# Kernel optimization log

Measured on AMD Instinct MI355X. Metric: run time of the kernel, lower is better.

## Reference

```python
import jax, jax.numpy as jnp
import numpy as np

DELTA_PULL = 0.5
DELTA_PUSH = 1.5
ALPHA, BETA, GAMMA = 1.0, 1.0, 0.001
M, E = 2_000_000, 32
NUM_IDS = 65  # labels 0..64; 0 = background


def setup_inputs() -> dict:
    key = jax.random.key(0)
    k1, k2 = jax.random.split(key)
    embeddings = jax.random.normal(k1, (M, E), dtype=jnp.float32)
    instance_labels = jax.random.randint(k2, (M,), 0, NUM_IDS, dtype=jnp.int64)
    return {"embeddings": embeddings, "instance_labels": instance_labels}


def reference(embeddings, instance_labels):
    # Foreground mask; background (label 0) points are excluded from every term.
    fg = instance_labels > 0
    labels = jnp.where(fg, instance_labels, 0).astype(jnp.int32)
    w = fg.astype(embeddings.dtype)  # [M]

    # Per-instance means via one fused segment-sum (replaces Python loop over ids).
    sums = jax.ops.segment_sum(embeddings * w[:, None], labels, num_segments=NUM_IDS)  # [C+1,E]
    counts = jax.ops.segment_sum(w, labels, num_segments=NUM_IDS)                       # [C+1]
    present = (counts > 0).at[0].set(False)  # slot 0 is background
    safe_counts = jnp.maximum(counts, 1.0)
    means = sums / safe_counts[:, None]  # [C+1,E]
    C = jnp.sum(present)
    Cf = jnp.maximum(C, 1).astype(embeddings.dtype)

    # Pull loss: per-point distance to own instance mean, hinged, per-instance mean, then mean over instances.
    diff_pt = embeddings - means[labels]
    d2_pt = jnp.sum(diff_pt * diff_pt, axis=1)
    dist_pt = jnp.sqrt(jnp.where(d2_pt > 0, d2_pt, 1.0))
    dist_pt = jnp.where(d2_pt > 0, dist_pt, 0.0)
    pull_pt = jnp.maximum(dist_pt - DELTA_PULL, 0.0) ** 2 * w
    pull_per_inst = jax.ops.segment_sum(pull_pt, labels, num_segments=NUM_IDS) / safe_counts
    pull_loss = jnp.sum(jnp.where(present, pull_per_inst, 0.0)) / Cf

    # Push loss: vectorized O(C^2) pairwise mean distances with upper-triangular mask.
    dm = means[:, None, :] - means[None, :, :]           # [C+1,C+1,E]
    d2 = jnp.sum(dm * dm, axis=-1)                        # [C+1,C+1]
    iu = jnp.triu(jnp.ones((NUM_IDS, NUM_IDS), bool), k=1)
    pairmask = iu & present[:, None] & present[None, :]
    pd = jnp.sqrt(jnp.where(pairmask, d2, 1.0))
    push = jnp.where(pairmask, jnp.maximum(2.0 * DELTA_PUSH - pd, 0.0) ** 2, 0.0)
    n_pairs = jnp.sum(pairmask)
    push_loss = jnp.where(
        n_pairs > 0,
        jnp.sum(push) / jnp.maximum(n_pairs, 1).astype(embeddings.dtype),
        0.0,
    )

    # Regularizer: mean norm of present instance means.
    mn2 = jnp.sum(means * means, axis=-1)
    mnorm = jnp.sqrt(jnp.where(present, mn2, 1.0))
    reg_loss = jnp.sum(jnp.where(present, mnorm, 0.0)) / Cf

    total = ALPHA * pull_loss + BETA * push_loss + GAMMA * reg_loss
    # If there are no foreground points, loss is 0 (matches torch early-return).
    total = jnp.where(C > 0, total, 0.0)
    return total
```

## Files before the change

### kernel.cpp

```cpp
#include <hip/hip_runtime.h>

#define NUM_IDS 65
#define EDIM 32
#define NSUM (NUM_IDS * EDIM)
#define NTOT (NSUM + NUM_IDS)
#define LPAD 33
#define R36 36
#define CP (NUM_IDS * R36)

#define WS_SUMS    0
#define WS_PULLACC 2148
#define WS_PART    2176

#define DPPI(x, ctrl) __builtin_amdgcn_update_dpp(0, (x), (ctrl), 0xF, 0xF, true)

__device__ __forceinline__ void gload4(const float4* p, float4& d) {
    asm volatile("global_load_dwordx4 %0, %1, off" : "=v"(d) : "v"(p));
}
__device__ __forceinline__ void gload1(const int* p, int& d) {
    asm volatile("global_load_dword %0, %1, off" : "=v"(d) : "v"(p));
}
__device__ __forceinline__ void waitN() {
    asm volatile("s_waitcnt vmcnt(4)" ::: "memory");
    __builtin_amdgcn_sched_barrier(0);
}
__device__ __forceinline__ void wait0() {
    asm volatile("s_waitcnt vmcnt(0)" ::: "memory");
    __builtin_amdgcn_sched_barrier(0);
}

__global__ void k0_zero(float* __restrict__ ws) {
    int i = blockIdx.x * 256 + threadIdx.x;
    if (i < NTOT) ws[WS_SUMS + i] = 0.f;
    if (i == 0) ws[WS_PULLACC] = 0.f;
}

__global__ __launch_bounds__(256) void k1_reduce(const float4* __restrict__ emb4,
                                                 const int* __restrict__ lab,
                                                 float* __restrict__ ws,
                                                 int M, int nb1, int nit, int atomic_mode) {
    __shared__ float ls[4 * CP];
    const int t = threadIdx.x;
    const int wave = t >> 6, lane = t & 63;
    const int s = lane & 7;
    const int c = lane >> 3;
    float* my = ls + wave * CP;
    for (int j = t; j < 4 * CP; j += 256) ls[j] = 0.f;
    __syncthreads();

    const long Mm1 = (long)M - 1;
    const long STR = (long)nb1 * 32;
    const long p0 = (long)blockIdx.x * 32 + wave * 8 + s;
    const int lp1 = lane + 1;
    int cntreg = 0;
    const int negkey = -64 - s;
    const int e1 = (s ^ 1) < s, e2 = (s ^ 2) < s, e3 = (s ^ 3) < s,
              e4 = (s ^ 4) < s, e5 = (s ^ 5) < s, e6 = (s ^ 6) < s, e7 = (s ^ 7) < s;

    auto ISSUE = [&](int j, int& L, float4& v) {
        long p = p0 + (long)j * STR;
        long pc = p < Mm1 ? p : Mm1;
        gload1(lab + pc, L);
        gload4(emb4 + pc * 8 + c, v);
    };
    auto PROC = [&](int j, int L, float4 v) {
        const bool inb = (p0 + (long)j * STR) < (long)M;
        const bool act = inb && (L > 0);
        int x0 = act ? L : negkey;
        int x1 = DPPI(x0, 0xB1);
        int x2 = DPPI(x0, 0x4E);
        int x3 = DPPI(x1, 0x4E);
        int x4 = DPPI(x0, 0x124);
        int x5 = DPPI(x1, 0x124);
        int x6 = DPPI(x2, 0x124);
        int x7 = DPPI(x3, 0x124);
        cntreg += (x0 == lp1) + (x1 == lp1) + (x2 == lp1) + (x3 == lp1)
                + (x4 == lp1) + (x5 == lp1) + (x6 == lp1) + (x7 == lp1);
        int ne = (e1 & (x1 == x0)) + (e2 & (x2 == x0)) + (e3 & (x3 == x0))
               + (e4 & (x4 == x0)) + (e5 & (x5 == x0)) + (e6 & (x6 == x0))
               + (e7 & (x7 == x0));
        const int off = (act ? L : 0) * R36 + c * 4;
        if (act && ne == 0) {
            float4 o = *(float4*)(my + off);
            o.x += v.x; o.y += v.y; o.z += v.z; o.w += v.w;
            *(float4*)(my + off) = o;
        }
        if (__ballot(act && ne > 0)) {
            #pragma unroll 1
            for (int r = 1; r < 8; ++r) {
                if (!__ballot(act && ne == r)) break;
                if (act && ne == r) {
                    float4 o = *(float4*)(my + off);
                    o.x += v.x; o.y += v.y; o.z += v.z; o.w += v.w;
                    *(float4*)(my + off) = o;
                }
            }
        }
    };

    int LA, LB, LC; float4 VA, VB, VC;
    ISSUE(0, LA, VA); ISSUE(1, LB, VB);
    for (int i = 0; i < nit; i += 3) {
        ISSUE(i + 2, LC, VC); waitN(); PROC(i, LA, VA);
        ISSUE(i + 3, LA, VA); waitN(); PROC(i + 1, LB, VB);
        ISSUE(i + 4, LB, VB); waitN(); PROC(i + 2, LC, VC);
    }
    wait0();

    my[lp1 * R36 + 32] += (float)cntreg;
    __syncthreads();

    for (int j = t; j < NTOT; j += 256) {
        int off = (j < NSUM) ? ((j >> 5) * R36 + (j & 31))
                             : ((j - NSUM) * R36 + 32);
        float v = ls[off] + ls[CP + off] + ls[2 * CP + off] + ls[3 * CP + off];
        if (atomic_mode) {
            if (v != 0.f) atomicAdd(&ws[WS_SUMS + j], v);
        } else {
            ws[WS_PART + (size_t)blockIdx.x * NTOT + j] = v;
        }
    }
}

__global__ __launch_bounds__(256) void k2_reduce_partials(float* __restrict__ ws, int nb1) {
    const int t = threadIdx.x;
    const int jl = t & 31, bl = t >> 5;
    const int j = blockIdx.x * 32 + jl;
    const float* part = ws + WS_PART;
    float acc = 0.f;
    if (j < NTOT) {
        int b = bl;
        for (; b + 56 < nb1; b += 64) {
            float v0 = part[(size_t)(b +  0) * NTOT + j];
            float v1 = part[(size_t)(b +  8) * NTOT + j];
            float v2 = part[(size_t)(b + 16) * NTOT + j];
            float v3 = part[(size_t)(b + 24) * NTOT + j];
            float v4 = part[(size_t)(b + 32) * NTOT + j];
            float v5 = part[(size_t)(b + 40) * NTOT + j];
            float v6 = part[(size_t)(b + 48) * NTOT + j];
            float v7 = part[(size_t)(b + 56) * NTOT + j];
            acc += ((v0 + v1) + (v2 + v3)) + ((v4 + v5) + (v6 + v7));
        }
        for (; b < nb1; b += 8) acc += part[(size_t)b * NTOT + j];
    }
    __shared__ float red[256];
    red[t] = acc;
    __syncthreads();
    for (int sd = 128; sd >= 32; sd >>= 1) {
        if (t < sd) red[t] += red[t + sd];
        __syncthreads();
    }
    if (t < 32) {
        int jj = blockIdx.x * 32 + t;
        if (jj < NTOT) ws[WS_SUMS + jj] = red[t];
    }
    if (blockIdx.x == 0 && t == 0) ws[WS_PULLACC] = 0.f;
}

__global__ __launch_bounds__(256) void k4_pull(const float4* __restrict__ emb4,
                                               const int* __restrict__ lab,
                                               float* __restrict__ ws,
                                               int M, int nb4) {
    __shared__ float lmean[NUM_IDS * LPAD];
    __shared__ float lcoef[NUM_IDS];
    __shared__ float lpull[NUM_IDS];
    __shared__ float red[NUM_IDS];
    const int t = threadIdx.x;
    for (int j = t; j < NSUM; j += 256) {
        int cc = j >> 5;
        lmean[cc * LPAD + (j & 31)] = ws[WS_SUMS + j] / fmaxf(ws[WS_SUMS + NSUM + cc], 1.f);
    }
    if (t < NUM_IDS) {
        float cv = ws[WS_SUMS + NSUM + t];
        lcoef[t] = (t > 0 && cv > 0.f) ? (1.f / fmaxf(cv, 1.f)) : 0.f;
        lpull[t] = 0.f;
    }
    __syncthreads();

    const int c = t & 7;
    const long stride = (long)nb4 * 32;
    const long start = (long)blockIdx.x * 32 + (t >> 3);

    auto LD = [&](long p, int& L, float4& v) {
        if (p < M) { L = lab[p]; v = emb4[p * 8 + c]; }
        else       { L = 0; v = make_float4(0.f, 0.f, 0.f, 0.f); }
    };
    auto PR = [&](int L, float4 v) {
        float d2 = 0.f;
        if (L > 0) {
            int bse = L * LPAD + c * 4;
            float dx = v.x - lmean[bse + 0];
            float dy = v.y - lmean[bse + 1];
            float dz = v.z - lmean[bse + 2];
            float dw = v.w - lmean[bse + 3];
            d2 = dx * dx + dy * dy + dz * dz + dw * dw;
        }
        d2 += __shfl_xor(d2, 1);
        d2 += __shfl_xor(d2, 2);
        d2 += __shfl_xor(d2, 4);
        if (c == 0 && L > 0 && d2 > 0.f) {
            float dist = sqrtf(d2);
            float h = fmaxf(dist - 0.5f, 0.f);
            atomicAdd(&lpull[L], h * h);
        }
    };

    int L0, L1;
    float4 v0, v1;
    long pA = start;
    LD(pA, L0, v0);
    while (pA < M) {
        const long pB = pA + stride;
        LD(pB, L1, v1);
        PR(L0, v0);
        const long pA2 = pB + stride;
        LD(pA2, L0, v0);
        PR(L1, v1);
        pA = pA2;
    }
    __syncthreads();
    if (t < NUM_IDS) red[t] = lpull[t] * lcoef[t];
    __syncthreads();
    if (t == 0) {
        float sacc = 0.f;
        for (int cc = 1; cc < NUM_IDS; ++cc) sacc += red[cc];
        atomicAdd(&ws[WS_PULLACC], sacc);
    }
}

__global__ __launch_bounds__(256) void k5_final(float* __restrict__ ws,
                                                float* __restrict__ out) {
    __shared__ float lmean[NUM_IDS * LPAD];
    __shared__ int   lpres[NUM_IDS];
    __shared__ float red[256];
    __shared__ float red2[256];
    const int t = threadIdx.x;

    if (t < NUM_IDS) {
        float cv = ws[WS_SUMS + NSUM + t];
        lpres[t] = (t > 0 && cv > 0.f) ? 1 : 0;
    }
    for (int j = t; j < NSUM; j += 256) {
        int cc = j >> 5;
        lmean[cc * LPAD + (j & 31)] = ws[WS_SUMS + j] / fmaxf(ws[WS_SUMS + NSUM + cc], 1.f);
    }
    __syncthreads();

    float psum = 0.f;
    for (int pi = t; pi < 2080; pi += 256) {
        int i = 0, rem = pi;
        while (rem >= NUM_IDS - 1 - i) { rem -= NUM_IDS - 1 - i; ++i; }
        int jj = i + 1 + rem;
        if (lpres[i] && lpres[jj]) {
            float d2 = 0.f;
            #pragma unroll
            for (int e = 0; e < EDIM; ++e) {
                float d = lmean[i * LPAD + e] - lmean[jj * LPAD + e];
                d2 += d * d;
            }
            float pd = sqrtf(d2);
            float h = fmaxf(3.0f - pd, 0.f);
            psum += h * h;
        }
    }
    float rsum = 0.f;
    if (t < NUM_IDS && lpres[t]) {
        float m2 = 0.f;
        #pragma unroll
        for (int e = 0; e < EDIM; ++e) { float m = lmean[t * LPAD + e]; m2 += m * m; }
        rsum = sqrtf(m2);
    }
    red[t] = psum; red2[t] = rsum;
    __syncthreads();
    for (int sd = 128; sd > 0; sd >>= 1) {
        if (t < sd) { red[t] += red[t + sd]; red2[t] += red2[t + sd]; }
        __syncthreads();
    }
    if (t == 0) {
        int C = 0;
        for (int cc = 1; cc < NUM_IDS; ++cc) C += lpres[cc];
        float Cf = fmaxf((float)C, 1.f);
        long np = (long)C * (C - 1) / 2;
        float push = (np > 0) ? red[0] / (float)np : 0.f;
        float reg  = red2[0] / Cf;
        float total = 0.f;
        if (C > 0) total = ws[WS_PULLACC] / Cf + push + 0.001f * reg;
        out[0] = total;
    }
}

extern "C" void kernel_launch(void* const* d_in, const int* in_sizes, int n_in,
                              void* d_out, int out_size, void* d_ws, size_t ws_size,
                              hipStream_t stream) {
    const float4* emb4 = (const float4*)d_in[0];
    const int* lab = (const int*)d_in[1];
    float* ws = (float*)d_ws;
    float* out = (float*)d_out;
    const int M = in_sizes[1];

    long ws_floats = (long)(ws_size / 4);
    long avail = ws_floats - WS_PART - 64;
    int nb1 = (int)(avail / NTOT);
    if (nb1 > 1024) nb1 = 1024;
    int atomic_mode = (nb1 < 8) ? 1 : 0;
    if (atomic_mode) {
        nb1 = 1024;
        k0_zero<<<dim3(9), dim3(256), 0, stream>>>(ws);
    }
    long str1 = (long)nb1 * 32;
    int nit1 = (int)((M + str1 - 1) / str1);
    nit1 = ((nit1 + 2) / 3) * 3;

    k1_reduce<<<dim3(nb1), dim3(256), 0, stream>>>(emb4, lab, ws, M, nb1, nit1, atomic_mode);
    if (!atomic_mode)
        k2_reduce_partials<<<dim3((NTOT + 31) / 32), dim3(256), 0, stream>>>(ws, nb1);
    const int nb4 = 2048;
    k4_pull<<<dim3(nb4), dim3(256), 0, stream>>>(emb4, lab, ws, M, nb4);
    k5_final<<<dim3(1), dim3(256), 0, stream>>>(ws, out);
}
```

Before: 135.3 us.

## Software-pipeline pull kernel with asm loads, DPP reduction and nontemporal hints

Rewrites the pull kernel's main loop as a three-deep software pipeline. Loads are issued with inline asm and explicit vmcnt waits, which replaces the compiler-scheduled two-stage loop with bounds branches. The 8-lane distance reduction moves from shfl_xor to DPP, and means are stored with stride 36 so each lane reads a float4 from LDS. Embedding loads in both streaming kernels gain the nt hint to reduce cache pollution. The trade-off is more register pressure, and nt may stop the second pass over the embeddings from reusing data left in cache by the first.

```diff
diff --git a/kernel.cpp b/kernel.cpp
--- a/kernel.cpp
+++ b/kernel.cpp
@@ -4,7 +4,6 @@
 #define EDIM 32
 #define NSUM (NUM_IDS * EDIM)
 #define NTOT (NSUM + NUM_IDS)
-#define LPAD 33
 #define R36 36
 #define CP (NUM_IDS * R36)
 
@@ -14,8 +13,8 @@
 
 #define DPPI(x, ctrl) __builtin_amdgcn_update_dpp(0, (x), (ctrl), 0xF, 0xF, true)
 
-__device__ __forceinline__ void gload4(const float4* p, float4& d) {
-    asm volatile("global_load_dwordx4 %0, %1, off" : "=v"(d) : "v"(p));
+__device__ __forceinline__ void gload4nt(const float4* p, float4& d) {
+    asm volatile("global_load_dwordx4 %0, %1, off nt" : "=v"(d) : "v"(p));
 }
 __device__ __forceinline__ void gload1(const int* p, int& d) {
     asm volatile("global_load_dword %0, %1, off" : "=v"(d) : "v"(p));
@@ -61,7 +60,7 @@
         long p = p0 + (long)j * STR;
         long pc = p < Mm1 ? p : Mm1;
         gload1(lab + pc, L);
-        gload4(emb4 + pc * 8 + c, v);
+        gload4nt(emb4 + pc * 8 + c, v);
     };
     auto PROC = [&](int j, int L, float4 v) {
         const bool inb = (p0 + (long)j * STR) < (long)M;
@@ -160,15 +159,17 @@
 __global__ __launch_bounds__(256) void k4_pull(const float4* __restrict__ emb4,
                                                const int* __restrict__ lab,
                                                float* __restrict__ ws,
-                                               int M, int nb4) {
-    __shared__ float lmean[NUM_IDS * LPAD];
+                                               int M, int nb4, int nit) {
+    __shared__ float lmean[NUM_IDS * R36];
     __shared__ float lcoef[NUM_IDS];
     __shared__ float lpull[NUM_IDS];
     __shared__ float red[NUM_IDS];
     const int t = threadIdx.x;
+    const int lane = t & 63;
+    const int s = lane >> 3, c = lane & 7;
     for (int j = t; j < NSUM; j += 256) {
         int cc = j >> 5;
-        lmean[cc * LPAD + (j & 31)] = ws[WS_SUMS + j] / fmaxf(ws[WS_SUMS + NSUM + cc], 1.f);
+        lmean[cc * R36 + (j & 31)] = ws[WS_SUMS + j] / fmaxf(ws[WS_SUMS + NSUM + cc], 1.f);
     }
     if (t < NUM_IDS) {
         float cv = ws[WS_SUMS + NSUM + t];
@@ -177,47 +178,42 @@
     }
     __syncthreads();
 
-    const int c = t & 7;
-    const long stride = (long)nb4 * 32;
-    const long start = (long)blockIdx.x * 32 + (t >> 3);
-
-    auto LD = [&](long p, int& L, float4& v) {
-        if (p < M) { L = lab[p]; v = emb4[p * 8 + c]; }
-        else       { L = 0; v = make_float4(0.f, 0.f, 0.f, 0.f); }
+    const long Mm1 = (long)M - 1;
+    const long STR = (long)nb4 * 32;
+    const long p0 = (long)blockIdx.x * 32 + (t >> 6) * 8 + s;
+
+    auto ISSUE = [&](int j, int& L, float4& v) {
+        long p = p0 + (long)j * STR;
+        long pc = p < Mm1 ? p : Mm1;
+        gload1(lab + pc, L);
+        gload4nt(emb4 + pc * 8 + c, v);
     };
-    auto PR = [&](int L, float4 v) {
-        float d2 = 0.f;
-        if (L > 0) {
-            int bse = L * LPAD + c * 4;
-            float dx = v.x - lmean[bse + 0];
-            float dy = v.y - lmean[bse + 1];
-            float dz = v.z - lmean[bse + 2];
-            float dw = v.w - lmean[bse + 3];
-            d2 = dx * dx + dy * dy + dz * dz + dw * dw;
-        }
-        d2 += __shfl_xor(d2, 1);
-        d2 += __shfl_xor(d2, 2);
-        d2 += __shfl_xor(d2, 4);
-        if (c == 0 && L > 0 && d2 > 0.f) {
+    auto PROC = [&](int j, int L, float4 v) {
+        const bool inb = (p0 + (long)j * STR) < (long)M;
+        const bool act = inb && (L > 0);
+        const float4 mu = *(const float4*)(lmean + L * R36 + c * 4);
+        float dx = v.x - mu.x, dy = v.y - mu.y, dz = v.z - mu.z, dw = v.w - mu.w;
+        float d2 = act ? (dx * dx + dy * dy + dz * dz + dw * dw) : 0.f;
+        int bb;
+        bb = DPPI(__float_as_int(d2), 0xB1); d2 += __int_as_float(bb);
+        bb = DPPI(__float_as_int(d2), 0x4E); d2 += __int_as_float(bb);
+        bb = DPPI(DPPI(__float_as_int(d2), 0x141), 0x1B);
+        d2 += __int_as_float(bb);
+        if (c == 0 && act && d2 > 0.f) {
             float dist = sqrtf(d2);
             float h = fmaxf(dist - 0.5f, 0.f);
             atomicAdd(&lpull[L], h * h);
         }
     };
 
-    int L0, L1;
-    float4 v0, v1;
-    long pA = start;
-    LD(pA, L0, v0);
-    while (pA < M) {
-        const long pB = pA + stride;
-        LD(pB, L1, v1);
-        PR(L0, v0);
-        const long pA2 = pB + stride;
-        LD(pA2, L0, v0);
-        PR(L1, v1);
-        pA = pA2;
-    }
+    int LA, LB, LC; float4 VA, VB, VC;
+    ISSUE(0, LA, VA); ISSUE(1, LB, VB);
+    for (int i = 0; i < nit; i += 3) {
+        ISSUE(i + 2, LC, VC); waitN(); PROC(i, LA, VA);
+        ISSUE(i + 3, LA, VA); waitN(); PROC(i + 1, LB, VB);
+        ISSUE(i + 4, LB, VB); waitN(); PROC(i + 2, LC, VC);
+    }
+    wait0();
     __syncthreads();
     if (t < NUM_IDS) red[t] = lpull[t] * lcoef[t];
     __syncthreads();
@@ -230,7 +226,7 @@
 
 __global__ __launch_bounds__(256) void k5_final(float* __restrict__ ws,
                                                 float* __restrict__ out) {
-    __shared__ float lmean[NUM_IDS * LPAD];
+    __shared__ float lmean[NUM_IDS * R36];
     __shared__ int   lpres[NUM_IDS];
     __shared__ float red[256];
     __shared__ float red2[256];
@@ -242,7 +238,7 @@
     }
     for (int j = t; j < NSUM; j += 256) {
         int cc = j >> 5;
-        lmean[cc * LPAD + (j & 31)] = ws[WS_SUMS + j] / fmaxf(ws[WS_SUMS + NSUM + cc], 1.f);
+        lmean[cc * R36 + (j & 31)] = ws[WS_SUMS + j] / fmaxf(ws[WS_SUMS + NSUM + cc], 1.f);
     }
     __syncthreads();
 
@@ -255,7 +251,7 @@
             float d2 = 0.f;
             #pragma unroll
             for (int e = 0; e < EDIM; ++e) {
-                float d = lmean[i * LPAD + e] - lmean[jj * LPAD + e];
+                float d = lmean[i * R36 + e] - lmean[jj * R36 + e];
                 d2 += d * d;
             }
             float pd = sqrtf(d2);
@@ -267,7 +263,7 @@
     if (t < NUM_IDS && lpres[t]) {
         float m2 = 0.f;
         #pragma unroll
-        for (int e = 0; e < EDIM; ++e) { float m = lmean[t * LPAD + e]; m2 += m * m; }
+        for (int e = 0; e < EDIM; ++e) { float m = lmean[t * R36 + e]; m2 += m * m; }
         rsum = sqrtf(m2);
     }
     red[t] = psum; red2[t] = rsum;
@@ -311,10 +307,14 @@
     int nit1 = (int)((M + str1 - 1) / str1);
     nit1 = ((nit1 + 2) / 3) * 3;
 
+    const int nb4 = 2048;
+    long str4 = (long)nb4 * 32;
+    int nit4 = (int)((M + str4 - 1) / str4);
+    nit4 = ((nit4 + 2) / 3) * 3;
+
     k1_reduce<<<dim3(nb1), dim3(256), 0, stream>>>(emb4, lab, ws, M, nb1, nit1, atomic_mode);
     if (!atomic_mode)
         k2_reduce_partials<<<dim3((NTOT + 31) / 32), dim3(256), 0, stream>>>(ws, nb1);
-    const int nb4 = 2048;
-    k4_pull<<<dim3(nb4), dim3(256), 0, stream>>>(emb4, lab, ws, M, nb4);
+    k4_pull<<<dim3(nb4), dim3(256), 0, stream>>>(emb4, lab, ws, M, nb4, nit4);
     k5_final<<<dim3(1), dim3(256), 0, stream>>>(ws, out);
 }
```

Measured after the change: 149.1 us. 10.2% more time.
